# Kernel optimization log

Measured on AMD Instinct MI355X. Metric: run time of the kernel, lower is better.

The kernel has to match this reference:

```python
import jax, jax.numpy as jnp
import numpy as np

EPS = 1e-6  # GLOBAL_EPS
D_QK = 192
ATTN_DIM = 768


def setup_inputs() -> dict:
    key = jax.random.key(0)
    ks = jax.random.split(key, 12)
    B, C, H, W = 16, 192, 56, 56
    d_qk, d_v = D_QK, 2 * D_QK
    attn_dim, inner = ATTN_DIM, d_v
    r = lambda k, s, sc=0.05: jax.random.normal(k, s, dtype=jnp.float32) * sc
    return {
        "x": jax.random.normal(ks[0], (B, C, H, W), dtype=jnp.float32),
        "proj_w": r(ks[1], (attn_dim, C)),          # 1x1 conv + BN folded
        "proj_b": r(ks[2], (attn_dim,)),
        "dwc_w": r(ks[3], (attn_dim, 1, 3, 3)),     # depthwise 3x3, BN folded
        "dwc_b": r(ks[4], (attn_dim,)),
        "g_w": r(ks[5], (inner, attn_dim)),          # ConvGate pointwise conv1d
        "g_b": r(ks[6], (inner,)),
        "an_w": 1.0 + r(ks[7], (inner,)),            # RMSNorm weight
        "sv": 1.0 + r(ks[8], (inner,)),              # Scale(inner, (1, inner, 1))
        "out_w": r(ks[9], (C, inner)),               # 1x1 conv + BN folded
        "out_b": r(ks[10], (C,)),
    }


def reference(x, proj_w, proj_b, dwc_w, dwc_b, g_w, g_b, an_w, sv, out_w, out_b):
    B, C, H, W = x.shape
    d_qk = D_QK
    # proj: ConvNorm 1x1 (conv + BN folded to affine)
    y = jnp.einsum("bchw,oc->bohw", x, proj_w) + proj_b[None, :, None, None]
    # dwc: RepConv depthwise 3x3 with residual (res=True)
    dw = jax.lax.conv_general_dilated(
        y, dwc_w, window_strides=(1, 1), padding="SAME",
        dimension_numbers=("NCHW", "OIHW", "NCHW"),
        feature_group_count=ATTN_DIM)
    y = dw + dwc_b[None, :, None, None] + y
    # flatten spatial -> tokens, split q/k/v along channels
    xs = y.reshape(B, ATTN_DIM, H * W)            # (B, attn_dim, N)
    q, k, v = xs[:, :d_qk], xs[:, d_qk:2 * d_qk], xs[:, 2 * d_qk:]
    # linear_attn: feature map = silu, scale = N**-0.5
    qf = jax.nn.silu(q)                            # (B, d_qk, N)
    kf = jax.nn.silu(k)
    N = H * W
    s = N ** -0.5
    # use_linear branch (N >> d): z = kT.mean(-2,True) @ q + eps ; attn = (v s)(kT s) q
    z = jnp.einsum("bd,bdn->bn", kf.mean(-1), qf)[:, None, :] + EPS  # (B, 1, N)
    vk = jnp.einsum("bvn,bdn->bvd", v * s, kf * s)  # (B, d_v, d_qk)
    attn = jnp.einsum("bvd,bdn->bvn", vk, qf) / z   # (B, d_v, N)
    # gate: pointwise conv1d on full projected features + sigmoid
    gate = jax.nn.sigmoid(jnp.einsum("bcn,oc->bon", xs, g_w) + g_b[None, :, None])
    attn = attn * gate
    # attn_norm (RMS over channels) + scale_v(v) residual
    rms = jnp.sqrt(jnp.mean(attn * attn, axis=1, keepdims=True) + EPS)
    attn = attn / rms * an_w[None, :, None] + v * sv[None, :, None]
    # out: ConvNorm 1x1 back to dim
    o = attn.reshape(B, -1, H, W)
    return jnp.einsum("bchw,oc->bohw", o, out_w) + out_b[None, :, None, None]
```

## Files before the change

kernel.cpp:

```cpp
#include <hip/hip_runtime.h>
#include <hip/hip_bf16.h>

typedef unsigned short u16;
typedef __attribute__((ext_vector_type(8))) short bf16x8;
typedef __attribute__((ext_vector_type(4))) float f32x4;

constexpr int B_ = 16, C_ = 192, H_ = 56, W_ = 56;
constexpr int N_ = H_ * W_;
constexpr int A_ = 768;
constexpr int Dq = 192;
constexpr int Vd = 384;
constexpr float EPSf = 1e-6f;

union U8 { bf16x8 v; u16 s[8]; unsigned u[4]; };

__device__ __forceinline__ float bits2f(u16 u) {
  return __uint_as_float(((unsigned)u) << 16);
}
__device__ __forceinline__ u16 f2bits(float f) {
  __hip_bfloat16 h = __float2bfloat16(f);
  u16 u;
  __builtin_memcpy(&u, &h, sizeof(u));
  return u;
}
__device__ __forceinline__ float silu_f(float v) { return v / (1.0f + __expf(-v)); }
__device__ __forceinline__ float sigm_f(float v) { return 1.0f / (1.0f + __expf(-v)); }

__device__ __forceinline__ f32x4 MFMA(bf16x8 a, bf16x8 b, f32x4 c) {
  return __builtin_amdgcn_mfma_f32_16x16x32_bf16(a, b, c, 0, 0, 0);
}
__device__ __forceinline__ int swz(int row) { return (row & 7) ^ ((row >> 3) & 7); }

__global__ __launch_bounds__(256) void k_prep(const float* __restrict__ pw,
                                              const float* __restrict__ gw,
                                              const float* __restrict__ ow,
                                              u16* __restrict__ pwb,
                                              u16* __restrict__ gwb,
                                              u16* __restrict__ owb) {
  const int bid = blockIdx.x;
  const size_t base = ((size_t)bid * 256 + threadIdx.x) * 8;
  const float* src;
  u16* dst;
  size_t off;
  if (bid < 72) { src = pw; dst = pwb; off = base; }
  else if (bid < 216) { src = gw; dst = gwb; off = base - 147456; }
  else { src = ow; dst = owb; off = base - 442368; }
  float4 v0 = *(const float4*)&src[off];
  float4 v1 = *(const float4*)&src[off + 4];
  U8 r;
  r.s[0] = f2bits(v0.x); r.s[1] = f2bits(v0.y); r.s[2] = f2bits(v0.z); r.s[3] = f2bits(v0.w);
  r.s[4] = f2bits(v1.x); r.s[5] = f2bits(v1.y); r.s[6] = f2bits(v1.z); r.s[7] = f2bits(v1.w);
  *(bf16x8*)&dst[off] = r.v;
}

__global__ __launch_bounds__(256) void k_proj(const float* __restrict__ x,
                                              const u16* __restrict__ pwb,
                                              const float* __restrict__ pb,
                                              u16* __restrict__ y0t) {
  const int n0 = blockIdx.x * 64;
  const int oy = blockIdx.y;
  const int b = blockIdx.z;
  __shared__ u16 Xt[64][200];
  __shared__ u16 Wa[256][32];
  const int t = threadIdx.x;
  const int lane = t & 63, wid = t >> 6;
  const int fr = lane & 15, fg = lane >> 4;

  {
    const int p = t & 31, co = t >> 5;
    const float* xb = x + (size_t)b * C_ * N_ + n0 + 2 * p;
#pragma unroll
    for (int rnd = 0; rnd < 3; ++rnd) {
      const int c0 = rnd * 64 + co * 8;
      float2 v[8];
#pragma unroll
      for (int i = 0; i < 8; ++i) v[i] = *(const float2*)&xb[(size_t)(c0 + i) * N_];
      U8 r0, r1;
#pragma unroll
      for (int i = 0; i < 8; ++i) { r0.s[i] = f2bits(v[i].x); r1.s[i] = f2bits(v[i].y); }
      *(bf16x8*)&Xt[2 * p][c0] = r0.v;
      *(bf16x8*)&Xt[2 * p + 1][c0] = r1.v;
    }
  }

  f32x4 acc[4][4];
#pragma unroll
  for (int mi = 0; mi < 4; ++mi)
#pragma unroll
    for (int ni = 0; ni < 4; ++ni) acc[mi][ni] = (f32x4){0.f, 0.f, 0.f, 0.f};

  const int orow_c = t >> 2, oct_c = t & 3;
  U8 wreg[4];
#pragma unroll
  for (int jj = 0; jj < 4; ++jj)
    wreg[jj].v = *(const bf16x8*)&pwb[(size_t)(oy * 256 + orow_c + 64 * jj) * C_ + oct_c * 8];

  for (int ks = 0; ks < 6; ++ks) {
    __syncthreads();
#pragma unroll
    for (int jj = 0; jj < 4; ++jj) {
      const int orow = orow_c + 64 * jj;
      const int sw = (orow >> 1) & 3;
      *(bf16x8*)&Wa[orow][(oct_c ^ sw) * 8] = wreg[jj].v;
    }
    __syncthreads();
    if (ks < 5) {
#pragma unroll
      for (int jj = 0; jj < 4; ++jj)
        wreg[jj].v = *(const bf16x8*)&pwb[(size_t)(oy * 256 + orow_c + 64 * jj) * C_ +
                                          (ks + 1) * 32 + oct_c * 8];
    }
    bf16x8 bfrag[4];
#pragma unroll
    for (int ni = 0; ni < 4; ++ni)
      bfrag[ni] = *(const bf16x8*)&Xt[ni * 16 + fr][ks * 32 + fg * 8];
    __builtin_amdgcn_s_setprio(1);
#pragma unroll
    for (int mi = 0; mi < 4; ++mi) {
      const int ar = wid * 64 + mi * 16 + fr;
      bf16x8 a = *(const bf16x8*)&Wa[ar][(fg ^ ((ar >> 1) & 3)) * 8];
#pragma unroll
      for (int ni = 0; ni < 4; ++ni) acc[mi][ni] = MFMA(a, bfrag[ni], acc[mi][ni]);
    }
    __builtin_amdgcn_s_setprio(0);
  }
#pragma unroll
  for (int mi = 0; mi < 4; ++mi) {
    const int o4 = oy * 256 + wid * 64 + mi * 16 + fg * 4;
    const float b0 = pb[o4], b1 = pb[o4 + 1], b2 = pb[o4 + 2], b3 = pb[o4 + 3];
#pragma unroll
    for (int ni = 0; ni < 4; ++ni) {
      const int n = n0 + ni * 16 + fr;
      ushort4 pk;
      pk.x = f2bits(acc[mi][ni][0] + b0);
      pk.y = f2bits(acc[mi][ni][1] + b1);
      pk.z = f2bits(acc[mi][ni][2] + b2);
      pk.w = f2bits(acc[mi][ni][3] + b3);
      *(ushort4*)&y0t[((size_t)b * N_ + n) * A_ + o4] = pk;
    }
  }
}

__global__ __launch_bounds__(256) void k_dwc(const u16* __restrict__ y0t,
                                             const float* __restrict__ cw,
                                             const float* __restrict__ cb,
                                             u16* __restrict__ yt) {
  const int pid = blockIdx.x;
  const int L = (pid & 7) * 336 + (pid >> 3);
  const int h = L % 56, at = (L / 56) % 3, b = L / 168;
  const int t = threadIdx.x;
  const int a = at * 256 + (t & 31) * 8;
  const int wl = t >> 5;
  float w9[9][8];
  float bias[8];
#pragma unroll
  for (int j = 0; j < 8; ++j) {
    bias[j] = cb[a + j];
#pragma unroll
    for (int k = 0; k < 9; ++k) w9[k][j] = cw[(a + j) * 9 + k];
  }
  const u16* src = y0t + (size_t)b * N_ * A_ + a;
  u16* dst = yt + (size_t)b * N_ * A_ + a;
  const bool hok0 = h > 0, hok2 = h < 55;
  for (int wc = 0; wc < 7; ++wc) {
    const int w = wc * 8 + wl;
    const bool wok0 = w > 0, wok2 = w < 55;
    U8 nb[9];
#pragma unroll
    for (int dh = -1; dh <= 1; ++dh) {
      const bool hok = (dh == -1) ? hok0 : ((dh == 1) ? hok2 : true);
#pragma unroll
      for (int dw = -1; dw <= 1; ++dw) {
        const int k = (dh + 1) * 3 + (dw + 1);
        const bool ok = hok && ((dw == -1) ? wok0 : ((dw == 1) ? wok2 : true));
        if (ok)
          nb[k].v = *(const bf16x8*)&src[(size_t)((h + dh) * 56 + (w + dw)) * A_];
        else
          nb[k].u[0] = nb[k].u[1] = nb[k].u[2] = nb[k].u[3] = 0u;
      }
    }
    U8 o;
#pragma unroll
    for (int j = 0; j < 8; ++j) {
      float s = bias[j] + bits2f(nb[4].s[j]);
#pragma unroll
      for (int k = 0; k < 9; ++k) s = fmaf(w9[k][j], bits2f(nb[k].s[j]), s);
      o.s[j] = f2bits(s);
    }
    *(bf16x8*)&dst[(size_t)(h * 56 + w) * A_] = o.v;
  }
}

__global__ __launch_bounds__(256) void k_kfmean(const u16* __restrict__ yt,
                                                float* __restrict__ kfp) {
  const int ns = blockIdx.x, dc = blockIdx.y, b = blockIdx.z;
  const int t = threadIdx.x;
  const int dq = t & 15, nw = t >> 4;
  const u16* p = yt + ((size_t)b * N_ + ns * 448 + nw) * A_ + 192 + dc * 64 + dq * 4;
  float s0 = 0, s1 = 0, s2 = 0, s3 = 0;
#pragma unroll 4
  for (int i = 0; i < 28; ++i) {
    ushort4 u = *(const ushort4*)&p[(size_t)i * 16 * A_];
    s0 += silu_f(bits2f(u.x));
    s1 += silu_f(bits2f(u.y));
    s2 += silu_f(bits2f(u.z));
    s3 += silu_f(bits2f(u.w));
  }
  __shared__ float red[16][65];
  red[nw][dq * 4 + 0] = s0;
  red[nw][dq * 4 + 1] = s1;
  red[nw][dq * 4 + 2] = s2;
  red[nw][dq * 4 + 3] = s3;
  __syncthreads();
  if (t < 64) {
    float s = 0;
#pragma unroll
    for (int i = 0; i < 16; ++i) s += red[i][t];
    kfp[((size_t)ns * B_ + b) * Dq + dc * 64 + t] = s * (1.0f / (float)N_);
  }
}

__global__ __launch_bounds__(256) void k_z(const u16* __restrict__ yt,
                                           const float* __restrict__ kfp,
                                           float* __restrict__ zinv) {
  const int b = blockIdx.y;
  const int n = blockIdx.x * 256 + threadIdx.x;
  __shared__ float kf[192];
  if (threadIdx.x < 192) {
    float s = 0;
#pragma unroll
    for (int ns = 0; ns < 7; ++ns) s += kfp[((size_t)ns * B_ + b) * Dq + threadIdx.x];
    kf[threadIdx.x] = s;
  }
  __syncthreads();
  if (n < N_) {
    const u16* p = yt + ((size_t)b * N_ + n) * A_;
    float z = 0;
#pragma unroll
    for (int j = 0; j < 24; ++j) {
      U8 u;
      u.v = *(const bf16x8*)&p[j * 8];
#pragma unroll
      for (int i = 0; i < 8; ++i) z = fmaf(kf[j * 8 + i], silu_f(bits2f(u.s[i])), z);
    }
    zinv[(size_t)b * N_ + n] = 1.0f / (z + EPSf);
  }
}

__global__ __launch_bounds__(256) void k_vk(const u16* __restrict__ yt,
                                            float* __restrict__ vkpart) {
  const int pid = blockIdx.x;
  const int L = (pid & 7) * 42 + (pid >> 3);
  const int ns = L % 7;
  const int vblk = (L / 7) % 3;
  const int b = L / 21;
  const int t = threadIdx.x;
  const int lane = t & 63, wid = t >> 6;
  const int fr = lane & 15, fg = lane >> 4;
  const int vbase = (wid >> 1) * 64, dbase = (wid & 1) * 96;

  __shared__ u16 T[320 * 64];
  unsigned* T32 = (unsigned*)T;

  const int oct0 = t & 7;
  const int pair = (t >> 3) & 31;
  const int nb0 = ns * 448;

  U8 pre[5][2];
  auto load_pre = [&](int n0) {
    const int n = nb0 + n0 + pair * 2;
#pragma unroll
    for (int j = 0; j < 5; ++j) {
      const int oct = oct0 + 8 * j;
      const u16* srcp;
      if (j < 3)
        srcp = yt + ((size_t)b * N_ + n) * A_ + 192 + oct * 8;
      else
        srcp = yt + ((size_t)b * N_ + n) * A_ + 384 + vblk * 128 + (oct - 24) * 8;
      pre[j][0].v = *(const bf16x8*)srcp;
      pre[j][1].v = *(const bf16x8*)(srcp + A_);
      if (j < 3) {
#pragma unroll
        for (int i = 0; i < 8; ++i) {
          pre[j][0].s[i] = f2bits(silu_f(bits2f(pre[j][0].s[i])));
          pre[j][1].s[i] = f2bits(silu_f(bits2f(pre[j][1].s[i])));
        }
      }
    }
  };

  f32x4 acc[4][6];
#pragma unroll
  for (int mi = 0; mi < 4; ++mi)
#pragma unroll
    for (int ni = 0; ni < 6; ++ni) acc[mi][ni] = (f32x4){0.f, 0.f, 0.f, 0.f};

  load_pre(0);
  for (int s = 0; s < 7; ++s) {
    __syncthreads();
#pragma unroll
    for (int j = 0; j < 5; ++j) {
      const int rowb = (oct0 + 8 * j) * 8;
#pragma unroll
      for (int i = 0; i < 8; ++i) {
        const int row = rowb + i;
        const int sw = swz(row);
        const unsigned val =
            ((unsigned)pre[j][0].s[i] & 0xffffu) | (((unsigned)pre[j][1].s[i]) << 16);
        T32[row * 32 + (pair ^ (sw << 2))] = val;
      }
    }
    __syncthreads();
    if (s < 6) load_pre((s + 1) * 64);
    __builtin_amdgcn_s_setprio(1);
#pragma unroll
    for (int kf2 = 0; kf2 < 2; ++kf2) {
      bf16x8 bfrag[6];
#pragma unroll
      for (int ni = 0; ni < 6; ++ni) {
        const int row = dbase + ni * 16 + fr;
        bfrag[ni] = *(const bf16x8*)&T[row * 64 + ((kf2 * 32 + fg * 8) ^ (swz(row) << 3))];
      }
#pragma unroll
      for (int mi = 0; mi < 4; ++mi) {
        const int row = 192 + vbase + mi * 16 + fr;
        bf16x8 a = *(const bf16x8*)&T[row * 64 + ((kf2 * 32 + fg * 8) ^ (swz(row) << 3))];
#pragma unroll
        for (int ni = 0; ni < 6; ++ni) acc[mi][ni] = MFMA(a, bfrag[ni], acc[mi][ni]);
      }
    }
    __builtin_amdgcn_s_setprio(0);
  }
  float* base = vkpart + (((size_t)ns * 16 + b) * 3 + vblk) * (128 * 192);
#pragma unroll
  for (int mi = 0; mi < 4; ++mi)
#pragma unroll
    for (int ni = 0; ni < 6; ++ni) {
      const int v = vbase + mi * 16 + fg * 4;
      const int d = dbase + ni * 16 + fr;
      float* o = base + (size_t)v * 192 + d;
      o[0] = acc[mi][ni][0];
      o[192] = acc[mi][ni][1];
      o[384] = acc[mi][ni][2];
      o[576] = acc[mi][ni][3];
    }
}

__global__ __launch_bounds__(256) void k_vkred(const float* __restrict__ vkpart,
                                               u16* __restrict__ vkb) {
  const size_t e = ((size_t)blockIdx.x * 256 + threadIdx.x) * 8;
  constexpr size_t NSSTRIDE = (size_t)16 * 3 * 128 * 192;
  float4 s0 = {0, 0, 0, 0}, s1 = {0, 0, 0, 0};
#pragma unroll
  for (int ns = 0; ns < 7; ++ns) {
    float4 a0 = *(const float4*)&vkpart[ns * NSSTRIDE + e];
    float4 a1 = *(const float4*)&vkpart[ns * NSSTRIDE + e + 4];
    s0.x += a0.x; s0.y += a0.y; s0.z += a0.z; s0.w += a0.w;
    s1.x += a1.x; s1.y += a1.y; s1.z += a1.z; s1.w += a1.w;
  }
  const float sc = 1.0f / (float)N_;
  U8 r;
  r.s[0] = f2bits(s0.x * sc); r.s[1] = f2bits(s0.y * sc);
  r.s[2] = f2bits(s0.z * sc); r.s[3] = f2bits(s0.w * sc);
  r.s[4] = f2bits(s1.x * sc); r.s[5] = f2bits(s1.y * sc);
  r.s[6] = f2bits(s1.z * sc); r.s[7] = f2bits(s1.w * sc);
  *(bf16x8*)&vkb[e] = r.v;
}

__global__ __launch_bounds__(256) void k_gateattn(const u16* __restrict__ yt,
                                                  const float* __restrict__ zinv,
                                                  const u16* __restrict__ vkb,
                                                  const u16* __restrict__ gwb,
                                                  const float* __restrict__ gb,
                                                  u16* __restrict__ attnt) {
  const int pid = blockIdx.x;
  const int L = (pid & 7) * 196 + (pid >> 3);
  const int vh = L & 1;
  const int n0 = ((L >> 1) % 49) * 64;
  const int b = L / 98;
  const int t = threadIdx.x;
  const int lane = t & 63, wid = t >> 6, wm = wid >> 1, wn = wid & 1;
  const int fr = lane & 15, fg = lane >> 4;
  __shared__ u16 T[256 * 64];
  __shared__ float zl[64];
  if (t < 64) zl[t] = zinv[(size_t)b * N_ + n0 + t];
  const u16* yb = yt + ((size_t)b * N_ + n0) * A_;
  const u16* wb0 = vkb + ((size_t)b * Vd + vh * 192) * 192;
  const u16* wb1 = gwb + (size_t)(vh * 192) * A_;

  const int oct = t & 7, rowb = t >> 3;
  U8 pre[8];
  auto loadPre = [&](int nit) {
    const int ks = (nit < 3) ? nit * 64 : (nit - 3) * 64;
    const u16* wsrc = (nit < 3) ? (wb0 + ks) : (wb1 + ks);
    const size_t wstr = (nit < 3) ? 192 : 768;
#pragma unroll
    for (int j = 0; j < 6; ++j)
      pre[j].v = *(const bf16x8*)&wsrc[(size_t)(rowb + 32 * j) * wstr + oct * 8];
#pragma unroll
    for (int j = 6; j < 8; ++j) {
      const int n = rowb + 32 * (j - 6);
      pre[j].v = *(const bf16x8*)&yb[(size_t)n * A_ + ks + oct * 8];
    }
  };

  f32x4 acc[6][2];
#pragma unroll
  for (int mi = 0; mi < 6; ++mi)
#pragma unroll
    for (int ni = 0; ni < 2; ++ni) acc[mi][ni] = (f32x4){0.f, 0.f, 0.f, 0.f};
  uint2 pp[6][2];

  loadPre(0);
  for (int it = 0; it < 15; ++it) {
    __syncthreads();
    const bool sl = (it < 3);
#pragma unroll
    for (int j = 0; j < 8; ++j) {
      const int r = rowb + 32 * j;
      U8 w = pre[j];
      if (sl && j >= 6) {
#pragma unroll
        for (int i = 0; i < 8; ++i) w.s[i] = f2bits(silu_f(bits2f(w.s[i])));
      }
      *(bf16x8*)&T[r * 64 + ((oct * 8) ^ (swz(r) << 3))] = w.v;
    }
    __syncthreads();
    if (it < 14) loadPre(it + 1);
    __builtin_amdgcn_s_setprio(1);
#pragma unroll
    for (int kf2 = 0; kf2 < 2; ++kf2) {
      bf16x8 bfr[2];
#pragma unroll
      for (int ni = 0; ni < 2; ++ni) {
        const int row = 192 + wn * 32 + ni * 16 + fr;
        bfr[ni] = *(const bf16x8*)&T[row * 64 + ((kf2 * 32 + fg * 8) ^ (swz(row) << 3))];
      }
#pragma unroll
      for (int mi = 0; mi < 6; ++mi) {
        const int row = wm * 96 + mi * 16 + fr;
        bf16x8 a = *(const bf16x8*)&T[row * 64 + ((kf2 * 32 + fg * 8) ^ (swz(row) << 3))];
        acc[mi][0] = MFMA(a, bfr[0], acc[mi][0]);
        acc[mi][1] = MFMA(a, bfr[1], acc[mi][1]);
      }
    }
    __builtin_amdgcn_s_setprio(0);
    if (it == 2) {
#pragma unroll
      for (int mi = 0; mi < 6; ++mi)
#pragma unroll
        for (int ni = 0; ni < 2; ++ni) {
          const float z = zl[wn * 32 + ni * 16 + fr];
          unsigned a0 = ((unsigned)f2bits(acc[mi][ni][0] * z) & 0xffffu) |
                        (((unsigned)f2bits(acc[mi][ni][1] * z) & 0xffffu) << 16);
          unsigned a1 = ((unsigned)f2bits(acc[mi][ni][2] * z) & 0xffffu) |
                        (((unsigned)f2bits(acc[mi][ni][3] * z) & 0xffffu) << 16);
          pp[mi][ni] = make_uint2(a0, a1);
          acc[mi][ni] = (f32x4){0.f, 0.f, 0.f, 0.f};
        }
    }
  }

#pragma unroll
  for (int mi = 0; mi < 6; ++mi) {
    const int vb = vh * 192 + wm * 96 + mi * 16 + fg * 4;
    const float g0 = gb[vb], g1 = gb[vb + 1], g2 = gb[vb + 2], g3 = gb[vb + 3];
#pragma unroll
    for (int ni = 0; ni < 2; ++ni) {
      const int n = n0 + wn * 32 + ni * 16 + fr;
      const uint2 p = pp[mi][ni];
      const float pv0 = bits2f((u16)(p.x & 0xffffu)), pv1 = bits2f((u16)(p.x >> 16));
      const float pv2 = bits2f((u16)(p.y & 0xffffu)), pv3 = bits2f((u16)(p.y >> 16));
      ushort4 o;
      o.x = f2bits(pv0 * sigm_f(acc[mi][ni][0] + g0));
      o.y = f2bits(pv1 * sigm_f(acc[mi][ni][1] + g1));
      o.z = f2bits(pv2 * sigm_f(acc[mi][ni][2] + g2));
      o.w = f2bits(pv3 * sigm_f(acc[mi][ni][3] + g3));
      *(ushort4*)&attnt[((size_t)b * N_ + n) * Vd + vb] = o;
    }
  }
}

__global__ __launch_bounds__(256) void k_out(const u16* __restrict__ attnt,
                                             const u16* __restrict__ yt,
                                             const u16* __restrict__ owb,
                                             const float* __restrict__ ob,
                                             const float* __restrict__ anw,
                                             const float* __restrict__ svw,
                                             float* __restrict__ out) {
  const int n0 = blockIdx.x * 64;
  const int b = blockIdx.y;
  __shared__ u16 T[256 * 64];
  __shared__ float anws[384], svws[384];
  __shared__ float red[64][4];
  __shared__ float rinv[64];
  const int t = threadIdx.x;
  const int lane = t & 63, wid = t >> 6, wm = wid >> 1, wn = wid & 1;
  const int fr = lane & 15, fg = lane >> 4;
  for (int i = t; i < 384; i += 256) {
    anws[i] = anw[i];
    svws[i] = svw[i];
  }
  {
    const int n = t >> 2, q = t & 3;
    const u16* ab = attnt + ((size_t)b * N_ + n0 + n) * Vd;
    float ss = 0.f;
#pragma unroll
    for (int i = 0; i < 4; ++i) {
      U8 u, u2, u3;
      u.v = *(const bf16x8*)&ab[(q + 4 * i) * 8 + 0];
      u2.v = *(const bf16x8*)&ab[(q + 4 * i) * 8 + 128];
      u3.v = *(const bf16x8*)&ab[(q + 4 * i) * 8 + 256];
#pragma unroll
      for (int k = 0; k < 8; ++k) {
        float f0 = bits2f(u.s[k]), f1 = bits2f(u2.s[k]), f2 = bits2f(u3.s[k]);
        ss = fmaf(f0, f0, ss);
        ss = fmaf(f1, f1, ss);
        ss = fmaf(f2, f2, ss);
      }
    }
    red[n][q] = ss;
  }
  __syncthreads();
  if (t < 64)
    rinv[t] = rsqrtf((red[t][0] + red[t][1] + red[t][2] + red[t][3]) * (1.0f / (float)Vd) + EPSf);

  const int oct = t & 7, rowb = t >> 3;
  U8 preW[6], preA[2], preV[2];
  auto loadPre = [&](int it) {
    const int ks = it * 64;
#pragma unroll
    for (int j = 0; j < 6; ++j)
      preW[j].v = *(const bf16x8*)&owb[(size_t)(rowb + 32 * j) * Vd + ks + oct * 8];
#pragma unroll
    for (int j = 0; j < 2; ++j) {
      const int n = rowb + 32 * j;
      preA[j].v = *(const bf16x8*)&attnt[((size_t)b * N_ + n0 + n) * Vd + ks + oct * 8];
      preV[j].v = *(const bf16x8*)&yt[((size_t)b * N_ + n0 + n) * A_ + 384 + ks + oct * 8];
    }
  };

  f32x4 acc[6][2];
#pragma unroll
  for (int mi = 0; mi < 6; ++mi)
#pragma unroll
    for (int ni = 0; ni < 2; ++ni) acc[mi][ni] = (f32x4){0.f, 0.f, 0.f, 0.f};

  loadPre(0);
  __syncthreads();
  for (int it = 0; it < 6; ++it) {
#pragma unroll
    for (int j = 0; j < 6; ++j) {
      const int r = rowb + 32 * j;
      *(bf16x8*)&T[r * 64 + ((oct * 8) ^ (swz(r) << 3))] = preW[j].v;
    }
#pragma unroll
    for (int j = 0; j < 2; ++j) {
      const int n = rowb + 32 * j;
      const int r = 192 + n;
      const float ri = rinv[n];
      const int col0 = it * 64 + oct * 8;
      U8 o;
#pragma unroll
      for (int k = 0; k < 8; ++k)
        o.s[k] = f2bits(bits2f(preA[j].s[k]) * ri * anws[col0 + k] +
                        bits2f(preV[j].s[k]) * svws[col0 + k]);
      *(bf16x8*)&T[r * 64 + ((oct * 8) ^ (swz(r) << 3))] = o.v;
    }
    __syncthreads();
    if (it < 5) loadPre(it + 1);
    __builtin_amdgcn_s_setprio(1);
#pragma unroll
    for (int kf2 = 0; kf2 < 2; ++kf2) {
      bf16x8 bfr[2];
#pragma unroll
      for (int ni = 0; ni < 2; ++ni) {
        const int row = 192 + wn * 32 + ni * 16 + fr;
        bfr[ni] = *(const bf16x8*)&T[row * 64 + ((kf2 * 32 + fg * 8) ^ (swz(row) << 3))];
      }
#pragma unroll
      for (int mi = 0; mi < 6; ++mi) {
        const int row = wm * 96 + mi * 16 + fr;
        bf16x8 a = *(const bf16x8*)&T[row * 64 + ((kf2 * 32 + fg * 8) ^ (swz(row) << 3))];
        acc[mi][0] = MFMA(a, bfr[0], acc[mi][0]);
        acc[mi][1] = MFMA(a, bfr[1], acc[mi][1]);
      }
    }
    __builtin_amdgcn_s_setprio(0);
    if (it < 5) __syncthreads();
  }
#pragma unroll
  for (int mi = 0; mi < 6; ++mi) {
    const int c = wm * 96 + mi * 16 + fg * 4;
    const float b0 = ob[c], b1 = ob[c + 1], b2 = ob[c + 2], b3 = ob[c + 3];
#pragma unroll
    for (int ni = 0; ni < 2; ++ni) {
      const int n = n0 + wn * 32 + ni * 16 + fr;
      float* o = out + ((size_t)b * C_ + c) * N_ + n;
      o[0 * N_] = acc[mi][ni][0] + b0;
      o[1 * N_] = acc[mi][ni][1] + b1;
      o[2 * N_] = acc[mi][ni][2] + b2;
      o[3 * N_] = acc[mi][ni][3] + b3;
    }
  }
}

extern "C" void kernel_launch(void* const* d_in, const int* in_sizes, int n_in,
                              void* d_out, int out_size, void* d_ws, size_t ws_size,
                              hipStream_t stream) {
  (void)in_sizes; (void)n_in; (void)out_size; (void)ws_size;
  const float* x = (const float*)d_in[0];
  const float* pw = (const float*)d_in[1];
  const float* pb = (const float*)d_in[2];
  const float* cw = (const float*)d_in[3];
  const float* cb = (const float*)d_in[4];
  const float* gw = (const float*)d_in[5];
  const float* gb = (const float*)d_in[6];
  const float* anw = (const float*)d_in[7];
  const float* svw = (const float*)d_in[8];
  const float* ow = (const float*)d_in[9];
  const float* ob = (const float*)d_in[10];
  float* out = (float*)d_out;

  char* ws = (char*)d_ws;
  const size_t szY = (size_t)B_ * N_ * A_ * 2;
  u16* y0t = (u16*)(ws);
  u16* attnt = (u16*)(ws);
  float* vkpart = (float*)(ws + 38535168);
  u16* vkb = (u16*)(ws + 71565312);
  u16* yt = (u16*)(ws + szY);
  char* ws2 = ws + 2 * szY;
  float* kfp = (float*)(ws2);
  float* zinv = (float*)(ws2 + 86016);
  u16* pwb = (u16*)(ws2 + 86016 + 200704);
  u16* gwb = (u16*)(ws2 + 86016 + 200704 + 294912);
  u16* owb = (u16*)(ws2 + 86016 + 200704 + 294912 + 589824);

  k_prep<<<dim3(252), 256, 0, stream>>>(pw, gw, ow, pwb, gwb, owb);
  k_proj<<<dim3(49, 3, 16), 256, 0, stream>>>(x, pwb, pb, y0t);
  k_dwc<<<dim3(2688), 256, 0, stream>>>(y0t, cw, cb, yt);
  k_kfmean<<<dim3(7, 3, 16), 256, 0, stream>>>(yt, kfp);
  k_z<<<dim3(13, 16), 256, 0, stream>>>(yt, kfp, zinv);
  k_vk<<<dim3(336), 256, 0, stream>>>(yt, vkpart);
  k_vkred<<<dim3(576), 256, 0, stream>>>(vkpart, vkb);
  k_gateattn<<<dim3(1568), 256, 0, stream>>>(yt, zinv, vkb, gwb, gb, attnt);
  k_out<<<dim3(49, 16), 256, 0, stream>>>(attnt, yt, owb, ob, anw, svw, out);
}
```

Measured before the change: 281.0 us.

## Double-buffer LDS tiles in gate-attention kernel to cut one barrier per step

Switches the k_gateattn shared-memory tile to two buffers. Each iteration writes the next stage into the other buffer while computing on the current one, and global prefetch now runs two stages ahead. This drops one of the two __syncthreads per iteration and is meant to hide LDS stores and global load latency behind the MFMA work. In exchange, LDS per block doubles to about 64KB, which can reduce how many blocks fit on a CU, and holding the prefetch registers longer raises register pressure.

```diff
diff --git a/kernel.cpp b/kernel.cpp
--- a/kernel.cpp
+++ b/kernel.cpp
@@ -381,7 +381,7 @@
   const int t = threadIdx.x;
   const int lane = t & 63, wid = t >> 6, wm = wid >> 1, wn = wid & 1;
   const int fr = lane & 15, fg = lane >> 4;
-  __shared__ u16 T[256 * 64];
+  __shared__ u16 T[2][256 * 64];
   __shared__ float zl[64];
   if (t < 64) zl[t] = zinv[(size_t)b * N_ + n0 + t];
   const u16* yb = yt + ((size_t)b * N_ + n0) * A_;
@@ -391,30 +391,27 @@
   const int oct = t & 7, rowb = t >> 3;
   U8 pre[8];
   auto loadPre = [&](int nit) {
-    const int ks = (nit < 3) ? nit * 64 : (nit - 3) * 64;
-    const u16* wsrc = (nit < 3) ? (wb0 + ks) : (wb1 + ks);
-    const size_t wstr = (nit < 3) ? 192 : 768;
-#pragma unroll
-    for (int j = 0; j < 6; ++j)
-      pre[j].v = *(const bf16x8*)&wsrc[(size_t)(rowb + 32 * j) * wstr + oct * 8];
-#pragma unroll
-    for (int j = 6; j < 8; ++j) {
-      const int n = rowb + 32 * (j - 6);
-      pre[j].v = *(const bf16x8*)&yb[(size_t)n * A_ + ks + oct * 8];
+    if (nit < 3) {
+      const int ks = nit * 64;
+#pragma unroll
+      for (int j = 0; j < 6; ++j)
+        pre[j].v = *(const bf16x8*)&wb0[(size_t)(rowb + 32 * j) * 192 + ks + oct * 8];
+#pragma unroll
+      for (int j = 6; j < 8; ++j)
+        pre[j].v = *(const bf16x8*)&yb[(size_t)(rowb + 32 * (j - 6)) * A_ + ks + oct * 8];
+    } else {
+      const int ks = (nit - 3) * 64;
+#pragma unroll
+      for (int j = 0; j < 6; ++j)
+        pre[j].v = *(const bf16x8*)&wb1[(size_t)(rowb + 32 * j) * A_ + ks + oct * 8];
+#pragma unroll
+      for (int j = 6; j < 8; ++j)
+        pre[j].v = *(const bf16x8*)&yb[(size_t)(rowb + 32 * (j - 6)) * A_ + ks + oct * 8];
     }
   };
-
-  f32x4 acc[6][2];
-#pragma unroll
-  for (int mi = 0; mi < 6; ++mi)
-#pragma unroll
-    for (int ni = 0; ni < 2; ++ni) acc[mi][ni] = (f32x4){0.f, 0.f, 0.f, 0.f};
-  uint2 pp[6][2];
-
-  loadPre(0);
-  for (int it = 0; it < 15; ++it) {
-    __syncthreads();
-    const bool sl = (it < 3);
+  auto writeStage = [&](int nit, int buf) {
+    const bool sl = (nit < 3);
+    u16* Tb = &T[buf][0];
 #pragma unroll
     for (int j = 0; j < 8; ++j) {
       const int r = rowb + 32 * j;
@@ -423,10 +420,27 @@
 #pragma unroll
         for (int i = 0; i < 8; ++i) w.s[i] = f2bits(silu_f(bits2f(w.s[i])));
       }
-      *(bf16x8*)&T[r * 64 + ((oct * 8) ^ (swz(r) << 3))] = w.v;
-    }
-    __syncthreads();
-    if (it < 14) loadPre(it + 1);
+      *(bf16x8*)&Tb[r * 64 + ((oct * 8) ^ (swz(r) << 3))] = w.v;
+    }
+  };
+
+  f32x4 acc[6][2];
+#pragma unroll
+  for (int mi = 0; mi < 6; ++mi)
+#pragma unroll
+    for (int ni = 0; ni < 2; ++ni) acc[mi][ni] = (f32x4){0.f, 0.f, 0.f, 0.f};
+  uint2 pp[6][2];
+
+  loadPre(0);
+  writeStage(0, 0);
+  loadPre(1);
+  __syncthreads();
+
+  for (int it = 0; it < 15; ++it) {
+    const int cur = it & 1;
+    if (it < 14) writeStage(it + 1, cur ^ 1);
+    if (it < 13) loadPre(it + 2);
+    const u16* Tb = &T[cur][0];
     __builtin_amdgcn_s_setprio(1);
 #pragma unroll
     for (int kf2 = 0; kf2 < 2; ++kf2) {
@@ -434,12 +448,12 @@
 #pragma unroll
       for (int ni = 0; ni < 2; ++ni) {
         const int row = 192 + wn * 32 + ni * 16 + fr;
-        bfr[ni] = *(const bf16x8*)&T[row * 64 + ((kf2 * 32 + fg * 8) ^ (swz(row) << 3))];
+        bfr[ni] = *(const bf16x8*)&Tb[row * 64 + ((kf2 * 32 + fg * 8) ^ (swz(row) << 3))];
       }
 #pragma unroll
       for (int mi = 0; mi < 6; ++mi) {
         const int row = wm * 96 + mi * 16 + fr;
-        bf16x8 a = *(const bf16x8*)&T[row * 64 + ((kf2 * 32 + fg * 8) ^ (swz(row) << 3))];
+        bf16x8 a = *(const bf16x8*)&Tb[row * 64 + ((kf2 * 32 + fg * 8) ^ (swz(row) << 3))];
         acc[mi][0] = MFMA(a, bfr[0], acc[mi][0]);
         acc[mi][1] = MFMA(a, bfr[1], acc[mi][1]);
       }
@@ -459,6 +473,7 @@
           acc[mi][ni] = (f32x4){0.f, 0.f, 0.f, 0.f};
         }
     }
+    __syncthreads();
   }
 
 #pragma unroll
```

Measured after the change: 264.3 us. 1.06x faster.
